# Kernel optimization log

Measured on AMD Instinct MI355X. Metric: run time of the kernel, lower is better.

## Reference

```python
import jax, jax.numpy as jnp
import numpy as np

SIGMA = 16
P = 2 * SIGMA + 1  # 33x33 patch
OUT = 128          # feature_extractor.output_size
DN = ('NCHW', 'OIHW', 'NCHW')


def setup_inputs() -> dict:
    key = jax.random.key(0)
    ks = jax.random.split(key, 10)
    B, K, H, W = 4, 64, 256, 256
    images_ground = jax.random.normal(ks[0], (B, 3, H, W), jnp.float32)
    images_satellite = jax.random.normal(ks[1], (B, 3, H, W), jnp.float32)
    # normalized keypoints kept in interior so sigma-window crops stay in-bounds
    keypoints_ground = 0.2 + 0.6 * jax.random.uniform(ks[2], (B, K, 2), jnp.float32)
    keypoints_satellite = 0.2 + 0.6 * jax.random.uniform(ks[3], (B, K, 2), jnp.float32)
    # small CNN feature extractor params (conv 3->32 s1, conv 32->64 s2, GAP, linear 64->OUT)
    w1 = jax.random.normal(ks[4], (32, 3, 3, 3), jnp.float32) * 0.1
    b1 = jnp.zeros((32,), jnp.float32)
    w2 = jax.random.normal(ks[5], (64, 32, 3, 3), jnp.float32) * 0.05
    b2 = jnp.zeros((64,), jnp.float32)
    wl = jax.random.normal(ks[6], (OUT, 64), jnp.float32) * 0.1
    bl = jnp.zeros((OUT,), jnp.float32)
    return dict(images_ground=images_ground, images_satellite=images_satellite,
                keypoints_ground=keypoints_ground, keypoints_satellite=keypoints_satellite,
                w1=w1, b1=b1, w2=w2, b2=b2, wl=wl, bl=bl, num_samples=K)


def _cnn(x, w1, b1, w2, b2, wl, bl):
    # x: [M, 3, P, P] -> [M, OUT]
    h = jax.lax.conv_general_dilated(x, w1, (1, 1), 'VALID', dimension_numbers=DN)
    h = jax.nn.relu(h + b1[None, :, None, None])
    h = jax.lax.conv_general_dilated(h, w2, (2, 2), 'VALID', dimension_numbers=DN)
    h = jax.nn.relu(h + b2[None, :, None, None])
    h = h.mean(axis=(2, 3))  # global average pool -> [M, 64]
    return h @ wl.T + bl


def _crop_all(images, kps_px):
    # images: [B,3,H,W]; kps_px: [N,2] pixel (x, y) coords -> patches [N,B,3,P,P]
    B = images.shape[0]
    hw = images.shape[-1]
    starts = jnp.clip(jnp.floor(kps_px).astype(jnp.int32) - SIGMA, 0, hw - P)
    def one(st):
        return jax.lax.dynamic_slice(images, (0, 0, st[1], st[0]), (B, 3, P, P))
    return jax.vmap(one)(starts)


def reference(images_ground, images_satellite, keypoints_ground, keypoints_satellite,
              w1, b1, w2, b2, wl, bl, num_samples):
    kg = (keypoints_ground * images_ground.shape[-1]).reshape(-1, 2)   # [N,2]
    ksat = (keypoints_satellite * images_satellite.shape[-1]).reshape(-1, 2)
    pg = _crop_all(images_ground, kg)        # [N,B,3,P,P]
    ps = _crop_all(images_satellite, ksat)   # [N,B,3,P,P]
    N, B = pg.shape[0], pg.shape[1]
    fg = _cnn(pg.reshape(N * B, 3, P, P), w1, b1, w2, b2, wl, bl)
    fs = _cnn(ps.reshape(N * B, 3, P, P), w1, b1, w2, b2, wl, bl)
    fg = fg.reshape(N, B, OUT).transpose(1, 0, 2)  # features_ground [B,N,OUT]
    fs = fs.reshape(N, B, OUT).transpose(1, 0, 2)
    return jnp.mean((fg - fs) ** 2)
```

## Files before the change

kernel.cpp:

```cpp
#include <hip/hip_runtime.h>

#define HW   256
#define Pp   33
#define PPAD 36
#define OUTF 128
#define SIG  16

#define KCP   40
#define PLROW (2 * 16 * KCP)
#define PLSZ  (6 * PLROW)
#define IMS   40

#define WS_W1FH 0
#define WS_W1FL 512
#define WS_BHI  1024
#define WS_BLO  10240
#define WS_WLT  19456

typedef __attribute__((ext_vector_type(8))) short v8s;
typedef __attribute__((ext_vector_type(4))) float f32x4;

__device__ __forceinline__ unsigned short f2bf_rne(float x) {
  unsigned u = __float_as_uint(x);
  unsigned r = (u + 0x7FFFu + ((u >> 16) & 1u)) >> 16;
  return (unsigned short)r;
}
__device__ __forceinline__ float bf2f(unsigned short h) {
  return __uint_as_float(((unsigned)h) << 16);
}

__global__ __launch_bounds__(256) void prep_kernel(
    const float* __restrict__ w1, const float* __restrict__ w2,
    const float* __restrict__ wl, float* __restrict__ ws,
    float* __restrict__ out) {
  int t = blockIdx.x * 256 + threadIdx.x;
  int stride = gridDim.x * 256;
  if (blockIdx.x == 0 && threadIdx.x == 0) out[0] = 0.0f;
  unsigned short* w1h = (unsigned short*)(ws + WS_W1FH);
  unsigned short* w1lo = (unsigned short*)(ws + WS_W1FL);
  for (int i = t; i < 1024; i += stride) {
    int j  = i & 7;
    int l  = (i >> 3) & 63;
    int nt = i >> 9;
    int k  = 8 * (l >> 4) + j;
    int ch = 16 * nt + (l & 15);
    float v = (k < 27) ? w1[ch * 27 + k] : 0.0f;
    unsigned short h = f2bf_rne(v);
    w1h[i]  = h;
    w1lo[i] = f2bf_rne(v - bf2f(h));
  }
  unsigned short* bhi = (unsigned short*)(ws + WS_BHI);
  unsigned short* blo = (unsigned short*)(ws + WS_BLO);
  for (int i = t; i < 18432; i += stride) {
    int j  = i & 7;
    int l  = (i >> 3) & 63;
    int w  = (i >> 9) & 3;
    int tp = i >> 11;
    int ch = w * 16 + (l & 15);
    int kc = ((l >> 4) << 3) + j;
    int ky = tp / 3, kx = tp - ky * 3;
    float v = w2[ch * 288 + kc * 9 + ky * 3 + kx];
    unsigned short h = f2bf_rne(v);
    bhi[i] = h;
    blo[i] = f2bf_rne(v - bf2f(h));
  }
  for (int i = t; i < 8192; i += stride) {
    int o = i & 127, ii = i >> 7;
    ws[WS_WLT + i] = wl[o * 64 + ii];
  }
}

__global__ __launch_bounds__(256) void patch_cnn_kernel(
    const float* __restrict__ imgG, const float* __restrict__ imgS,
    const float* __restrict__ kpG,  const float* __restrict__ kpS,
    const float* __restrict__ b1g,  const float* __restrict__ b2g,
    const float* __restrict__ blg,  const float* __restrict__ ws,
    float* __restrict__ out) {
  __shared__ __align__(16) unsigned short patch[3 * Pp * PPAD];
  __shared__ __align__(16) unsigned short imcol[2][32 * IMS];
  __shared__ __align__(16) unsigned short hiP[PLSZ];
  __shared__ float gapv[64];
  __shared__ float fstash[OUTF];
  __shared__ float lred[4];

  const int bid  = blockIdx.x;
  const int n    = bid >> 2;
  const int b    = bid & 3;
  const int tid  = threadIdx.x;
  const int wave = tid >> 6;
  const int lane = tid & 63;

  const int m16 = lane & 15;
  const int qq  = lane >> 4;
  const int mt  = wave & 1;
  const int nt  = wave >> 1;

  const int bm = tid & 31;
  const int kq = tid >> 5;
  int  boff[4];
  bool bval[4];
#pragma unroll
  for (int j = 0; j < 4; ++j) {
    int k = 4 * kq + j;
    bval[j] = (k < 27);
    int kk = bval[j] ? k : 0;
    int ci = kk / 9, r2 = kk - ci * 9, ky = r2 / 3, kx = r2 - ky * 3;
    boff[j] = (ci * Pp + ky) * PPAD + bm + kx;
  }

  const v8s w1hF = ((const v8s*)((const unsigned short*)(ws + WS_W1FH)))[nt * 64 + lane];
  const v8s w1lF = ((const v8s*)((const unsigned short*)(ws + WS_W1FL)))[nt * 64 + lane];
  const float b1v = b1g[nt * 16 + m16];

  const v8s* bhW = (const v8s*)((const unsigned short*)(ws + WS_BHI)) + (wave * 64 + lane);
  const v8s* blW = (const v8s*)((const unsigned short*)(ws + WS_BLO)) + (wave * 64 + lane);
  const float b2v = b2g[wave * 16 + m16];

  auto build_row = [&](int r, int ibuf) {
    unsigned short h[4];
#pragma unroll
    for (int j = 0; j < 4; ++j)
      h[j] = bval[j] ? patch[boff[j] + r * PPAD] : (unsigned short)0;
    unsigned w0 = (unsigned)h[0] | ((unsigned)h[1] << 16);
    unsigned w1_ = (unsigned)h[2] | ((unsigned)h[3] << 16);
    *(uint2*)&imcol[ibuf][bm * IMS + 4 * kq] = make_uint2(w0, w1_);
  };

  auto conv1_row = [&](int ibuf, int sl) {
    v8s af = *(const v8s*)&imcol[ibuf][(16 * mt + m16) * IMS + 8 * qq];
    f32x4 a1 = {0.f, 0.f, 0.f, 0.f};
    a1 = __builtin_amdgcn_mfma_f32_16x16x32_bf16(af, w1hF, a1, 0, 0, 0);
    a1 = __builtin_amdgcn_mfma_f32_16x16x32_bf16(af, w1lF, a1, 0, 0, 0);
#pragma unroll
    for (int rg = 0; rg < 4; ++rg) {
      int x = 16 * mt + 4 * qq + rg;
      float f = fmaxf(a1[rg] + b1v, 0.f);
      hiP[((sl * 2 + (x & 1)) * 16 + (x >> 1)) * KCP + 16 * nt + m16] = f2bf_rne(f);
    }
  };

  auto produce_pair = [&](int r0) {
    const int rB = min(r0 + 1, 30);
    int s0p = r0 % 6;
    int s1p = s0p + 1; if (s1p >= 6) s1p -= 6;
    __syncthreads();
    build_row(r0, 0);
    build_row(rB, 1);
    __syncthreads();
    conv1_row(0, s0p);
    conv1_row(1, s1p);
  };

  float dd = 0.0f;

#pragma unroll 1
  for (int side = 0; side < 2; ++side) {
    const float* img = side ? imgS : imgG;
    const float* kp  = side ? kpS : kpG;

    int sx = (int)floorf(kp[n * 2 + 0] * 256.0f) - SIG;
    int sy = (int)floorf(kp[n * 2 + 1] * 256.0f) - SIG;
    sx = min(max(sx, 0), HW - Pp);
    sy = min(max(sy, 0), HW - Pp);

    for (int i = tid; i < (3 * Pp * PPAD) / 2; i += 256) {
      int e  = 2 * i;
      int ci = e / (Pp * PPAD);
      int r2 = e - ci * (Pp * PPAD);
      int r  = r2 / PPAD;
      int cc = r2 - r * PPAD;
      float vx = 0.f, vy = 0.f;
      const float* rowp = &img[((b * 3 + ci) * HW + (sy + r)) * HW + sx];
      if (cc < 32) { float2 v = *(const float2*)(rowp + cc); vx = v.x; vy = v.y; }
      else if (cc == 32) { vx = rowp[32]; }
      unsigned pk = (unsigned)f2bf_rne(vx) | ((unsigned)f2bf_rne(vy) << 16);
      *(unsigned*)&patch[e] = pk;
    }
    produce_pair(0);
    produce_pair(2);

    float gapAcc = 0.0f;
    int s0 = 0;
#pragma unroll 1
    for (int y2 = 0; y2 < 15; ++y2) {
      __syncthreads();
      f32x4 acc = {0.f, 0.f, 0.f, 0.f};
#pragma unroll
      for (int ky = 0; ky < 3; ++ky) {
        int sk = s0 + ky; if (sk >= 6) sk -= 6;
#pragma unroll
        for (int kx = 0; kx < 3; ++kx) {
          const int p = kx & 1;
          int cp = m16 + (kx >> 1); if (cp > 15) cp = 15;
          const int idx = ((sk * 2 + p) * 16 + cp) * KCP + qq * 8;
          v8s ah = *(const v8s*)&hiP[idx];
          const int tp = ky * 3 + kx;
          v8s bh = bhW[tp * 256];
          v8s bl = blW[tp * 256];
          acc = __builtin_amdgcn_mfma_f32_16x16x32_bf16(ah, bh, acc, 0, 0, 0);
          acc = __builtin_amdgcn_mfma_f32_16x16x32_bf16(ah, bl, acc, 0, 0, 0);
        }
      }
      {
        float s = fmaxf(acc.x + b2v, 0.f) + fmaxf(acc.y + b2v, 0.f) +
                  fmaxf(acc.z + b2v, 0.f);
        if (qq < 3) s += fmaxf(acc.w + b2v, 0.f);
        gapAcc += s;
      }
      const int r0 = 2 * y2 + 4;
      if (r0 <= 30) produce_pair(r0);
      s0 += 2; if (s0 >= 6) s0 -= 6;
    }

    gapAcc += __shfl_down(gapAcc, 32, 64);
    gapAcc += __shfl_down(gapAcc, 16, 64);
    if (lane < 16) gapv[wave * 16 + m16] = gapAcc * (1.0f / 225.0f);
    __syncthreads();

    if (tid < OUTF) {
      float f = blg[tid];
#pragma unroll 8
      for (int i = 0; i < 64; ++i) f = fmaf(gapv[i], ws[WS_WLT + i * OUTF + tid], f);
      if (side == 0) fstash[tid] = f;
      else { float d = f - fstash[tid]; dd = d * d; }
    }
    __syncthreads();
  }

  dd += __shfl_down(dd, 32, 64);
  dd += __shfl_down(dd, 16, 64);
  dd += __shfl_down(dd, 8, 64);
  dd += __shfl_down(dd, 4, 64);
  dd += __shfl_down(dd, 2, 64);
  dd += __shfl_down(dd, 1, 64);
  if (lane == 0) lred[wave] = dd;
  __syncthreads();
  if (tid == 0) {
    float s = (lred[0] + lred[1]) + (lred[2] + lred[3]);
    atomicAdd(out, s * (1.0f / 131072.0f));
  }
}

extern "C" void kernel_launch(void* const* d_in, const int* in_sizes, int n_in,
                              void* d_out, int out_size, void* d_ws, size_t ws_size,
                              hipStream_t stream) {
  const float* imgG = (const float*)d_in[0];
  const float* imgS = (const float*)d_in[1];
  const float* kpG  = (const float*)d_in[2];
  const float* kpS  = (const float*)d_in[3];
  const float* w1   = (const float*)d_in[4];
  const float* b1   = (const float*)d_in[5];
  const float* w2   = (const float*)d_in[6];
  const float* b2   = (const float*)d_in[7];
  const float* wl   = (const float*)d_in[8];
  const float* bl   = (const float*)d_in[9];
  float* ws  = (float*)d_ws;
  float* out = (float*)d_out;

  hipLaunchKernelGGL(prep_kernel, dim3(32), dim3(256), 0, stream, w1, w2, wl, ws, out);
  hipLaunchKernelGGL(patch_cnn_kernel, dim3(1024), dim3(256), 0, stream,
                     imgG, imgS, kpG, kpS, b1, b2, bl, ws, out);
}
```

Before: 154.7 us.

## Split ground/satellite sides across blocks and move linear+loss to separate kernel

```diff
diff --git a/kernel.cpp b/kernel.cpp
--- a/kernel.cpp
+++ b/kernel.cpp
@@ -16,6 +16,7 @@
 #define WS_BHI  1024
 #define WS_BLO  10240
 #define WS_WLT  19456
+#define WS_GAPS 27648
 
 typedef __attribute__((ext_vector_type(8))) short v8s;
 typedef __attribute__((ext_vector_type(4))) float f32x4;
@@ -74,18 +75,16 @@
     const float* __restrict__ imgG, const float* __restrict__ imgS,
     const float* __restrict__ kpG,  const float* __restrict__ kpS,
     const float* __restrict__ b1g,  const float* __restrict__ b2g,
-    const float* __restrict__ blg,  const float* __restrict__ ws,
-    float* __restrict__ out) {
+    float* __restrict__ ws) {
   __shared__ __align__(16) unsigned short patch[3 * Pp * PPAD];
   __shared__ __align__(16) unsigned short imcol[2][32 * IMS];
   __shared__ __align__(16) unsigned short hiP[PLSZ];
-  __shared__ float gapv[64];
-  __shared__ float fstash[OUTF];
-  __shared__ float lred[4];
 
   const int bid  = blockIdx.x;
-  const int n    = bid >> 2;
-  const int b    = bid & 3;
+  const int side = bid & 1;
+  const int nb   = bid >> 1;
+  const int n    = nb >> 2;
+  const int b    = nb & 3;
   const int tid  = threadIdx.x;
   const int wave = tid >> 6;
   const int lane = tid & 63;
@@ -139,104 +138,130 @@
     }
   };
 
-  auto produce_pair = [&](int r0) {
-    const int rB = min(r0 + 1, 30);
-    int s0p = r0 % 6;
-    int s1p = s0p + 1; if (s1p >= 6) s1p -= 6;
+  auto ldA = [&](int sk, int kx) -> v8s {
+    const int p = kx & 1;
+    int cp = m16 + (kx >> 1); if (cp > 15) cp = 15;
+    return *(const v8s*)&hiP[((sk * 2 + p) * 16 + cp) * KCP + qq * 8];
+  };
+
+  const float* img = side ? imgS : imgG;
+  const float* kp  = side ? kpS : kpG;
+
+  int sx = (int)floorf(kp[n * 2 + 0] * 256.0f) - SIG;
+  int sy = (int)floorf(kp[n * 2 + 1] * 256.0f) - SIG;
+  sx = min(max(sx, 0), HW - Pp);
+  sy = min(max(sy, 0), HW - Pp);
+
+  for (int i = tid; i < (3 * Pp * PPAD) / 2; i += 256) {
+    int e  = 2 * i;
+    int ci = e / (Pp * PPAD);
+    int r2 = e - ci * (Pp * PPAD);
+    int r  = r2 / PPAD;
+    int cc = r2 - r * PPAD;
+    float vx = 0.f, vy = 0.f;
+    const float* rowp = &img[((b * 3 + ci) * HW + (sy + r)) * HW + sx];
+    if (cc < 32) { float2 v = *(const float2*)(rowp + cc); vx = v.x; vy = v.y; }
+    else if (cc == 32) { vx = rowp[32]; }
+    unsigned pk = (unsigned)f2bf_rne(vx) | ((unsigned)f2bf_rne(vy) << 16);
+    *(unsigned*)&patch[e] = pk;
+  }
+  __syncthreads();
+  build_row(0, 0); build_row(1, 1);
+  __syncthreads();
+  conv1_row(0, 0); conv1_row(1, 1);
+  __syncthreads();
+  build_row(2, 0); build_row(3, 1);
+  __syncthreads();
+  conv1_row(0, 2); conv1_row(1, 3);
+
+  float gapAcc = 0.0f;
+  int s0 = 0;
+  v8s c0, c1, c2;
+
+#pragma unroll 1
+  for (int y2 = 0; y2 < 15; ++y2) {
     __syncthreads();
-    build_row(r0, 0);
-    build_row(rB, 1);
+    if (y2 == 0) { c0 = ldA(0, 0); c1 = ldA(0, 1); c2 = ldA(0, 2); }
+    f32x4 acc = {0.f, 0.f, 0.f, 0.f};
+    acc = __builtin_amdgcn_mfma_f32_16x16x32_bf16(c0, bhW[0 * 256], acc, 0, 0, 0);
+    acc = __builtin_amdgcn_mfma_f32_16x16x32_bf16(c0, blW[0 * 256], acc, 0, 0, 0);
+    acc = __builtin_amdgcn_mfma_f32_16x16x32_bf16(c1, bhW[1 * 256], acc, 0, 0, 0);
+    acc = __builtin_amdgcn_mfma_f32_16x16x32_bf16(c1, blW[1 * 256], acc, 0, 0, 0);
+    acc = __builtin_amdgcn_mfma_f32_16x16x32_bf16(c2, bhW[2 * 256], acc, 0, 0, 0);
+    acc = __builtin_amdgcn_mfma_f32_16x16x32_bf16(c2, blW[2 * 256], acc, 0, 0, 0);
+    {
+      int sk1 = s0 + 1; if (sk1 >= 6) sk1 -= 6;
+      v8s a0 = ldA(sk1, 0), a1 = ldA(sk1, 1), a2 = ldA(sk1, 2);
+      acc = __builtin_amdgcn_mfma_f32_16x16x32_bf16(a0, bhW[3 * 256], acc, 0, 0, 0);
+      acc = __builtin_amdgcn_mfma_f32_16x16x32_bf16(a0, blW[3 * 256], acc, 0, 0, 0);
+      acc = __builtin_amdgcn_mfma_f32_16x16x32_bf16(a1, bhW[4 * 256], acc, 0, 0, 0);
+      acc = __builtin_amdgcn_mfma_f32_16x16x32_bf16(a1, blW[4 * 256], acc, 0, 0, 0);
+      acc = __builtin_amdgcn_mfma_f32_16x16x32_bf16(a2, bhW[5 * 256], acc, 0, 0, 0);
+      acc = __builtin_amdgcn_mfma_f32_16x16x32_bf16(a2, blW[5 * 256], acc, 0, 0, 0);
+    }
+    {
+      int sk2 = s0 + 2; if (sk2 >= 6) sk2 -= 6;
+      c0 = ldA(sk2, 0); c1 = ldA(sk2, 1); c2 = ldA(sk2, 2);
+      acc = __builtin_amdgcn_mfma_f32_16x16x32_bf16(c0, bhW[6 * 256], acc, 0, 0, 0);
+      acc = __builtin_amdgcn_mfma_f32_16x16x32_bf16(c0, blW[6 * 256], acc, 0, 0, 0);
+      acc = __builtin_amdgcn_mfma_f32_16x16x32_bf16(c1, bhW[7 * 256], acc, 0, 0, 0);
+      acc = __builtin_amdgcn_mfma_f32_16x16x32_bf16(c1, blW[7 * 256], acc, 0, 0, 0);
+      acc = __builtin_amdgcn_mfma_f32_16x16x32_bf16(c2, bhW[8 * 256], acc, 0, 0, 0);
+      acc = __builtin_amdgcn_mfma_f32_16x16x32_bf16(c2, blW[8 * 256], acc, 0, 0, 0);
+    }
+
+    const int r0 = 2 * y2 + 4;
+    if (r0 <= 30) { build_row(r0, 0); build_row(min(r0 + 1, 30), 1); }
     __syncthreads();
-    conv1_row(0, s0p);
-    conv1_row(1, s1p);
-  };
-
-  float dd = 0.0f;
-
-#pragma unroll 1
-  for (int side = 0; side < 2; ++side) {
-    const float* img = side ? imgS : imgG;
-    const float* kp  = side ? kpS : kpG;
-
-    int sx = (int)floorf(kp[n * 2 + 0] * 256.0f) - SIG;
-    int sy = (int)floorf(kp[n * 2 + 1] * 256.0f) - SIG;
-    sx = min(max(sx, 0), HW - Pp);
-    sy = min(max(sy, 0), HW - Pp);
-
-    for (int i = tid; i < (3 * Pp * PPAD) / 2; i += 256) {
-      int e  = 2 * i;
-      int ci = e / (Pp * PPAD);
-      int r2 = e - ci * (Pp * PPAD);
-      int r  = r2 / PPAD;
-      int cc = r2 - r * PPAD;
-      float vx = 0.f, vy = 0.f;
-      const float* rowp = &img[((b * 3 + ci) * HW + (sy + r)) * HW + sx];
-      if (cc < 32) { float2 v = *(const float2*)(rowp + cc); vx = v.x; vy = v.y; }
-      else if (cc == 32) { vx = rowp[32]; }
-      unsigned pk = (unsigned)f2bf_rne(vx) | ((unsigned)f2bf_rne(vy) << 16);
-      *(unsigned*)&patch[e] = pk;
-    }
-    produce_pair(0);
-    produce_pair(2);
-
-    float gapAcc = 0.0f;
-    int s0 = 0;
-#pragma unroll 1
-    for (int y2 = 0; y2 < 15; ++y2) {
-      __syncthreads();
-      f32x4 acc = {0.f, 0.f, 0.f, 0.f};
-#pragma unroll
-      for (int ky = 0; ky < 3; ++ky) {
-        int sk = s0 + ky; if (sk >= 6) sk -= 6;
-#pragma unroll
-        for (int kx = 0; kx < 3; ++kx) {
-          const int p = kx & 1;
-          int cp = m16 + (kx >> 1); if (cp > 15) cp = 15;
-          const int idx = ((sk * 2 + p) * 16 + cp) * KCP + qq * 8;
-          v8s ah = *(const v8s*)&hiP[idx];
-          const int tp = ky * 3 + kx;
-          v8s bh = bhW[tp * 256];
-          v8s bl = blW[tp * 256];
-          acc = __builtin_amdgcn_mfma_f32_16x16x32_bf16(ah, bh, acc, 0, 0, 0);
-          acc = __builtin_amdgcn_mfma_f32_16x16x32_bf16(ah, bl, acc, 0, 0, 0);
-        }
-      }
-      {
-        float s = fmaxf(acc.x + b2v, 0.f) + fmaxf(acc.y + b2v, 0.f) +
-                  fmaxf(acc.z + b2v, 0.f);
-        if (qq < 3) s += fmaxf(acc.w + b2v, 0.f);
-        gapAcc += s;
-      }
-      const int r0 = 2 * y2 + 4;
-      if (r0 <= 30) produce_pair(r0);
-      s0 += 2; if (s0 >= 6) s0 -= 6;
-    }
-
-    gapAcc += __shfl_down(gapAcc, 32, 64);
-    gapAcc += __shfl_down(gapAcc, 16, 64);
-    if (lane < 16) gapv[wave * 16 + m16] = gapAcc * (1.0f / 225.0f);
-    __syncthreads();
-
-    if (tid < OUTF) {
-      float f = blg[tid];
+    if (r0 <= 30) {
+      int sl = r0 % 6;
+      conv1_row(0, sl); conv1_row(1, sl + 1);
+    }
+
+    {
+      float s = fmaxf(acc.x + b2v, 0.f) + fmaxf(acc.y + b2v, 0.f) +
+                fmaxf(acc.z + b2v, 0.f);
+      if (qq < 3) s += fmaxf(acc.w + b2v, 0.f);
+      gapAcc += s;
+    }
+    s0 += 2; if (s0 >= 6) s0 -= 6;
+  }
+
+  gapAcc += __shfl_down(gapAcc, 32, 64);
+  gapAcc += __shfl_down(gapAcc, 16, 64);
+  if (lane < 16)
+    ws[WS_GAPS + (nb * 2 + side) * 64 + wave * 16 + m16] = gapAcc * (1.0f / 225.0f);
+}
+
+__global__ __launch_bounds__(128) void loss_kernel(
+    const float* __restrict__ ws, const float* __restrict__ blg,
+    float* __restrict__ out) {
+  __shared__ float sh[128];
+  __shared__ float wred[2];
+  const int p = blockIdx.x;
+  const int t = threadIdx.x;
+  sh[t] = ws[WS_GAPS + p * 128 + t];
+  __syncthreads();
+  float fG = blg[t];
 #pragma unroll 8
-      for (int i = 0; i < 64; ++i) f = fmaf(gapv[i], ws[WS_WLT + i * OUTF + tid], f);
-      if (side == 0) fstash[tid] = f;
-      else { float d = f - fstash[tid]; dd = d * d; }
-    }
-    __syncthreads();
-  }
-
+  for (int i = 0; i < 64; ++i)
+    fG = fmaf(sh[i], ws[WS_WLT + i * OUTF + t], fG);
+  float fS = blg[t];
+#pragma unroll 8
+  for (int i = 0; i < 64; ++i)
+    fS = fmaf(sh[64 + i], ws[WS_WLT + i * OUTF + t], fS);
+  float d = fS - fG;
+  float dd = d * d;
   dd += __shfl_down(dd, 32, 64);
   dd += __shfl_down(dd, 16, 64);
   dd += __shfl_down(dd, 8, 64);
   dd += __shfl_down(dd, 4, 64);
   dd += __shfl_down(dd, 2, 64);
   dd += __shfl_down(dd, 1, 64);
-  if (lane == 0) lred[wave] = dd;
-  __syncthreads();
-  if (tid == 0) {
-    float s = (lred[0] + lred[1]) + (lred[2] + lred[3]);
+  if ((t & 63) == 0) wred[t >> 6] = dd;
+  __syncthreads();
+  if (t == 0) {
+    float s = (wred[0] + wred[1]) + (0.0f + 0.0f);
     atomicAdd(out, s * (1.0f / 131072.0f));
   }
 }
@@ -258,6 +283,7 @@
   float* out = (float*)d_out;
 
   hipLaunchKernelGGL(prep_kernel, dim3(32), dim3(256), 0, stream, w1, w2, wl, ws, out);
-  hipLaunchKernelGGL(patch_cnn_kernel, dim3(1024), dim3(256), 0, stream,
-                     imgG, imgS, kpG, kpS, b1, b2, bl, ws, out);
-}
+  hipLaunchKernelGGL(patch_cnn_kernel, dim3(2048), dim3(256), 0, stream,
+                     imgG, imgS, kpG, kpS, b1, b2, ws);
+  hipLaunchKernelGGL(loss_kernel, dim3(1024), dim3(128), 0, stream, ws, bl, out);
+}
```

Result: slower. 173.4 us (+12.1%).

## Compute two conv2 output rows per iteration with an 8-row conv1 ring

Applied to the files above, without the earlier changes.

```diff
diff --git a/kernel.cpp b/kernel.cpp
--- a/kernel.cpp
+++ b/kernel.cpp
@@ -8,7 +8,7 @@
 
 #define KCP   40
 #define PLROW (2 * 16 * KCP)
-#define PLSZ  (6 * PLROW)
+#define PLSZ  (8 * PLROW)
 #define IMS   40
 
 #define WS_W1FH 0
@@ -77,7 +77,7 @@
     const float* __restrict__ blg,  const float* __restrict__ ws,
     float* __restrict__ out) {
   __shared__ __align__(16) unsigned short patch[3 * Pp * PPAD];
-  __shared__ __align__(16) unsigned short imcol[2][32 * IMS];
+  __shared__ __align__(16) unsigned short imcol[4][32 * IMS];
   __shared__ __align__(16) unsigned short hiP[PLSZ];
   __shared__ float gapv[64];
   __shared__ float fstash[OUTF];
@@ -139,17 +139,22 @@
     }
   };
 
-  auto produce_pair = [&](int r0) {
-    const int rB = min(r0 + 1, 30);
-    int s0p = r0 % 6;
-    int s1p = s0p + 1; if (s1p >= 6) s1p -= 6;
-    __syncthreads();
-    build_row(r0, 0);
-    build_row(rB, 1);
-    __syncthreads();
-    conv1_row(0, s0p);
-    conv1_row(1, s1p);
+  auto ldA = [&](int sk, int kx) -> v8s {
+    const int p = kx & 1;
+    int cp = m16 + (kx >> 1); if (cp > 15) cp = 15;
+    return *(const v8s*)&hiP[((sk * 2 + p) * 16 + cp) * KCP + qq * 8];
   };
+
+#define TAP2(tp, aA, aB)                                                      \
+  { v8s bh_ = bhW[(tp) * 256]; v8s bl_ = blW[(tp) * 256];                     \
+    accA = __builtin_amdgcn_mfma_f32_16x16x32_bf16(aA, bh_, accA, 0, 0, 0);   \
+    accB = __builtin_amdgcn_mfma_f32_16x16x32_bf16(aB, bh_, accB, 0, 0, 0);   \
+    accA = __builtin_amdgcn_mfma_f32_16x16x32_bf16(aA, bl_, accA, 0, 0, 0);   \
+    accB = __builtin_amdgcn_mfma_f32_16x16x32_bf16(aB, bl_, accB, 0, 0, 0); }
+#define TAP1(tp, aa)                                                          \
+  { v8s bh_ = bhW[(tp) * 256]; v8s bl_ = blW[(tp) * 256];                     \
+    acc = __builtin_amdgcn_mfma_f32_16x16x32_bf16(aa, bh_, acc, 0, 0, 0);     \
+    acc = __builtin_amdgcn_mfma_f32_16x16x32_bf16(aa, bl_, acc, 0, 0, 0); }
 
   float dd = 0.0f;
 
@@ -176,40 +181,78 @@
       unsigned pk = (unsigned)f2bf_rne(vx) | ((unsigned)f2bf_rne(vy) << 16);
       *(unsigned*)&patch[e] = pk;
     }
-    produce_pair(0);
-    produce_pair(2);
+    __syncthreads();
+    build_row(0, 0); build_row(1, 1); build_row(2, 2); build_row(3, 3);
+    __syncthreads();
+    conv1_row(0, 0); conv1_row(1, 1); conv1_row(2, 2); conv1_row(3, 3);
+    __syncthreads();
+    build_row(4, 0); build_row(5, 1);
+    __syncthreads();
+    conv1_row(0, 4); conv1_row(1, 5);
 
     float gapAcc = 0.0f;
-    int s0 = 0;
+
 #pragma unroll 1
-    for (int y2 = 0; y2 < 15; ++y2) {
+    for (int i = 0; i < 7; ++i) {
+      __syncthreads();
+      const int s0 = (4 * i)     & 7;
+      const int s1 = (4 * i + 1) & 7;
+      const int s2 = (4 * i + 2) & 7;
+      const int s3 = (4 * i + 3) & 7;
+      const int s4 = (4 * i + 4) & 7;
+      f32x4 accA = {0.f, 0.f, 0.f, 0.f};
+      f32x4 accB = {0.f, 0.f, 0.f, 0.f};
+      v8s sh0 = ldA(s2, 0), sh1 = ldA(s2, 1), sh2 = ldA(s2, 2);
+      {
+        v8s a0 = ldA(s0, 0), a1 = ldA(s0, 1), a2 = ldA(s0, 2);
+        TAP2(0, a0, sh0); TAP2(1, a1, sh1); TAP2(2, a2, sh2);
+      }
+      {
+        v8s a0 = ldA(s1, 0), a1 = ldA(s1, 1), a2 = ldA(s1, 2);
+        v8s b0 = ldA(s3, 0), b1 = ldA(s3, 1), b2 = ldA(s3, 2);
+        TAP2(3, a0, b0); TAP2(4, a1, b1); TAP2(5, a2, b2);
+      }
+      {
+        v8s b0 = ldA(s4, 0), b1 = ldA(s4, 1), b2 = ldA(s4, 2);
+        TAP2(6, sh0, b0); TAP2(7, sh1, b1); TAP2(8, sh2, b2);
+      }
+
+      const int r0 = 4 * i + 6;
+      if (r0     <= 30) build_row(r0,     0);
+      if (r0 + 1 <= 30) build_row(r0 + 1, 1);
+      if (r0 + 2 <= 30) build_row(r0 + 2, 2);
+      if (r0 + 3 <= 30) build_row(r0 + 3, 3);
+      __syncthreads();
+      if (r0     <= 30) conv1_row(0, r0 & 7);
+      if (r0 + 1 <= 30) conv1_row(1, (r0 + 1) & 7);
+      if (r0 + 2 <= 30) conv1_row(2, (r0 + 2) & 7);
+      if (r0 + 3 <= 30) conv1_row(3, (r0 + 3) & 7);
+
+      {
+        float sA = fmaxf(accA.x + b2v, 0.f) + fmaxf(accA.y + b2v, 0.f) +
+                   fmaxf(accA.z + b2v, 0.f);
+        if (qq < 3) sA += fmaxf(accA.w + b2v, 0.f);
+        gapAcc += sA;
+        float sB = fmaxf(accB.x + b2v, 0.f) + fmaxf(accB.y + b2v, 0.f) +
+                   fmaxf(accB.z + b2v, 0.f);
+        if (qq < 3) sB += fmaxf(accB.w + b2v, 0.f);
+        gapAcc += sB;
+      }
+    }
+
+    {
       __syncthreads();
       f32x4 acc = {0.f, 0.f, 0.f, 0.f};
-#pragma unroll
-      for (int ky = 0; ky < 3; ++ky) {
-        int sk = s0 + ky; if (sk >= 6) sk -= 6;
-#pragma unroll
-        for (int kx = 0; kx < 3; ++kx) {
-          const int p = kx & 1;
-          int cp = m16 + (kx >> 1); if (cp > 15) cp = 15;
-          const int idx = ((sk * 2 + p) * 16 + cp) * KCP + qq * 8;
-          v8s ah = *(const v8s*)&hiP[idx];
-          const int tp = ky * 3 + kx;
-          v8s bh = bhW[tp * 256];
-          v8s bl = blW[tp * 256];
-          acc = __builtin_amdgcn_mfma_f32_16x16x32_bf16(ah, bh, acc, 0, 0, 0);
-          acc = __builtin_amdgcn_mfma_f32_16x16x32_bf16(ah, bl, acc, 0, 0, 0);
-        }
-      }
-      {
-        float s = fmaxf(acc.x + b2v, 0.f) + fmaxf(acc.y + b2v, 0.f) +
-                  fmaxf(acc.z + b2v, 0.f);
-        if (qq < 3) s += fmaxf(acc.w + b2v, 0.f);
-        gapAcc += s;
-      }
-      const int r0 = 2 * y2 + 4;
-      if (r0 <= 30) produce_pair(r0);
-      s0 += 2; if (s0 >= 6) s0 -= 6;
+      v8s a0 = ldA(4, 0), a1 = ldA(4, 1), a2 = ldA(4, 2);
+      TAP1(0, a0); TAP1(1, a1); TAP1(2, a2);
+      v8s c0 = ldA(5, 0), c1 = ldA(5, 1), c2 = ldA(5, 2);
+      TAP1(3, c0); TAP1(4, c1); TAP1(5, c2);
+      v8s e0 = ldA(6, 0), e1 = ldA(6, 1), e2 = ldA(6, 2);
+      TAP1(6, e0); TAP1(7, e1); TAP1(8, e2);
+      float s = fmaxf(acc.x + b2v, 0.f) + fmaxf(acc.y + b2v, 0.f) +
+                fmaxf(acc.z + b2v, 0.f);
+      if (qq < 3) s += fmaxf(acc.w + b2v, 0.f);
+      gapAcc += s;
     }
 
     gapAcc += __shfl_down(gapAcc, 32, 64);
```

After: 149.5 us. 3.4% less time.
